# Kernel tuning notes

Measured on AMD Instinct MI355X. Metric: run time of the kernel, lower is better.

## Reference

```python
import jax, jax.numpy as jnp
import numpy as np

B, S, D = 4, 2048, 768
H, E = 12, 64  # num_heads, head_size


def setup_inputs() -> dict:
    key = jax.random.key(0)
    ks = jax.random.split(key, 9)
    sd = 1.0 / np.sqrt(D)
    return {
        "x": jax.random.normal(ks[0], (B, S, D), dtype=jnp.float32),
        "Wq": jax.random.normal(ks[1], (H, D, E), dtype=jnp.float32) * sd,
        "bq": jax.random.normal(ks[2], (H, E), dtype=jnp.float32) * 0.02,
        "Wk": jax.random.normal(ks[3], (H, D, E), dtype=jnp.float32) * sd,
        "bk": jax.random.normal(ks[4], (H, E), dtype=jnp.float32) * 0.02,
        "Wv": jax.random.normal(ks[5], (H, D, E), dtype=jnp.float32) * sd,
        "bv": jax.random.normal(ks[6], (H, E), dtype=jnp.float32) * 0.02,
        "Wp": jax.random.normal(ks[7], (H * E, D), dtype=jnp.float32) * sd,
        "bp": jax.random.normal(ks[8], (D,), dtype=jnp.float32) * 0.02,
    }


def reference(x, Wq, bq, Wk, bk, Wv, bv, Wp, bp):
    # Batched multi-head QKV projections (replaces per-head Python loop)
    q = jnp.einsum("bsd,hde->bhse", x, Wq) + bq[None, :, None, :]
    k = jnp.einsum("bsd,hde->bhse", x, Wk) + bk[None, :, None, :]
    v = jnp.einsum("bsd,hde->bhse", x, Wv) + bv[None, :, None, :]
    scale = 1.0 / jnp.sqrt(jnp.asarray(E, dtype=x.dtype))
    # Full materialized attention matrix [B,H,S,S] as in the original module
    wei = jnp.einsum("bhqe,bhke->bhqk", q, k) * scale
    wei = jax.nn.softmax(wei, axis=-1)  # dropout=0 (eval) => identity
    out = jnp.einsum("bhqk,bhke->bhqe", wei, v)  # [B,H,S,E]
    # concat heads in head order then output projection
    out = out.transpose(0, 2, 1, 3).reshape(B, S, H * E)
    return out @ Wp + bp
```

## Files before the change

### kernel.cpp

```cpp
#include <hip/hip_runtime.h>
#include <cstddef>
#include <cstdint>

#define NB 4
#define NH 12
#define SQ 2048
#define DM 768
#define EH 64
#define MTOT (NB*SQ)
#define NQKV (NH*3*EH)

typedef __attribute__((ext_vector_type(8))) short short8;
typedef __attribute__((ext_vector_type(4))) float floatx4;

#define QSCALE 0.18033688011112042f

__device__ __forceinline__ unsigned short f2bf(float f) {
    unsigned int u = __float_as_uint(f);
    u += 0x7fffu + ((u >> 16) & 1u);
    return (unsigned short)(u >> 16);
}

#if __has_builtin(__builtin_amdgcn_exp2f)
__device__ __forceinline__ float fast_exp2(float x) { return __builtin_amdgcn_exp2f(x); }
#else
__device__ __forceinline__ float fast_exp2(float x) { return exp2f(x); }
#endif

#if __has_builtin(__builtin_amdgcn_cvt_pk_bf16_f32)
typedef __attribute__((ext_vector_type(2))) __bf16 bf16x2_t;
__device__ __forceinline__ unsigned int pack_bf16(float lo, float hi) {
    bf16x2_t v = __builtin_amdgcn_cvt_pk_bf16_f32(lo, hi);
    return __builtin_bit_cast(unsigned int, v);
}
#else
__device__ __forceinline__ unsigned int pack_bf16(float lo, float hi) {
    unsigned int u0 = __float_as_uint(lo) + 0x8000u;
    unsigned int u1 = __float_as_uint(hi) + 0x8000u;
    return __builtin_amdgcn_perm(u1, u0, 0x07060302u);
}
#endif
__device__ __forceinline__ short8 pack8(float a0,float a1,float a2,float a3,
                                        float b0,float b1,float b2,float b3) {
    union { unsigned int u[4]; short8 s; } cv;
    cv.u[0] = pack_bf16(a0, a1);
    cv.u[1] = pack_bf16(a2, a3);
    cv.u[2] = pack_bf16(b0, b1);
    cv.u[3] = pack_bf16(b2, b3);
    return cv.s;
}
__device__ __forceinline__ void gl_lds16(const void* g, void* l) {
    __builtin_amdgcn_global_load_lds(
        (const __attribute__((address_space(1))) unsigned int*)g,
        (__attribute__((address_space(3))) unsigned int*)l, 16, 0, 0);
}

#define CVT_A 1572864
#define CVT_BIAS (CVT_A + 576)
#define NCVT ((CVT_BIAS + 255) / 256)
__global__ __launch_bounds__(256) void convert_all(
    const float* __restrict__ x,
    const float* __restrict__ Wq, const float* __restrict__ bq,
    const float* __restrict__ Wk, const float* __restrict__ bk,
    const float* __restrict__ Wv, const float* __restrict__ bv,
    const float* __restrict__ Wp,
    unsigned short* __restrict__ Xb, unsigned short* __restrict__ Wt,
    unsigned short* __restrict__ Wpt, float* __restrict__ bias_all)
{
    __shared__ unsigned short T[64][66];
    if (blockIdx.x < NCVT) {
        int t = blockIdx.x * 256 + threadIdx.x;
        if (t < CVT_A) {
            float4 v = ((const float4*)x)[t];
            ushort4 r; r.x = f2bf(v.x); r.y = f2bf(v.y); r.z = f2bf(v.z); r.w = f2bf(v.w);
            ((ushort4*)Xb)[t] = r;
        } else if (t < CVT_BIAS) {
            int u = (t - CVT_A) * 4;
            #pragma unroll
            for (int j = 0; j < 4; j++) {
                int n = u + j;
                int h = n / 192, rr = n % 192, wsel = rr >> 6, e = rr & 63;
                const float* bs = (wsel == 0) ? bq : ((wsel == 1) ? bk : bv);
                bias_all[n] = bs[h * EH + e] * ((wsel == 0) ? QSCALE : 1.0f);
            }
        }
        return;
    }
    const int bid = blockIdx.x - NCVT;
    const int t = threadIdx.x;
    const int rr = t >> 2;
    const int c4 = (t & 3) * 16;

    const float* src; int sstride; unsigned short* dst; float sc; int kt;
    if (bid < 432) {
        int j = bid / 12; kt = bid % 12;
        int h = j / 3, wsel = j % 3;
        const float* W = (wsel == 0) ? Wq : ((wsel == 1) ? Wk : Wv);
        src = W + (size_t)h * DM * EH;
        sstride = EH;
        dst = Wt + (size_t)(h * 192 + wsel * 64) * DM;
        sc = (wsel == 0) ? QSCALE : 1.0f;
    } else {
        int u = bid - 432;
        int ni = u / 12; kt = u % 12;
        src = Wp + ni * 64;
        sstride = DM;
        dst = Wpt + (size_t)(ni * 64) * DM;
        sc = 1.0f;
    }

    const float* s = src + (size_t)(kt * 64 + rr) * sstride + c4;
    #pragma unroll
    for (int j = 0; j < 16; j++)
        T[c4 + j][rr] = f2bf(s[j] * sc);
    __syncthreads();
    uint4 d0 = *(uint4*)&T[rr][c4];
    uint4 d1 = *(uint4*)&T[rr][c4 + 8];
    *(uint4*)&dst[(size_t)rr * DM + kt * 64 + c4]     = d0;
    *(uint4*)&dst[(size_t)rr * DM + kt * 64 + c4 + 8] = d1;
}

__global__ __launch_bounds__(256, 4) void qkv_mfma(
    const unsigned short* __restrict__ Xb, const unsigned short* __restrict__ Wt,
    const float* __restrict__ bias_all,
    unsigned short* __restrict__ Qo, unsigned short* __restrict__ Kf,
    unsigned short* __restrict__ Vf)
{
    __shared__ __align__(16) unsigned short SM[16384];
    unsigned short* const As0 = SM;
    unsigned short* const Bs0 = SM + 8192;
    const int tid = threadIdx.x;
    const int w = tid >> 6, lane = tid & 63;
    const int l15 = lane & 15, quad = lane >> 4;
    const int wm = w & 1, wn = w >> 1;
    const int lid = blockIdx.x + gridDim.x * blockIdx.y;
    const int xcd = lid & 7, pos = lid >> 3;
    const int bx = xcd * 8 + (pos & 7);
    const int by = pos >> 3;
    const int m0 = bx * 128, n0 = by * 128;
    const int srow = w * 32 + (lane >> 2);
    const int pchunk = lane & 3;

    floatx4 acc[4][4];
    #pragma unroll
    for (int i = 0; i < 4; i++)
        #pragma unroll
        for (int j = 0; j < 4; j++) acc[i][j] = 0;

    #pragma unroll
    for (int c = 0; c < 2; c++) {
        int mr = srow + c * 16;
        int j = (pchunk - (mr >> 1)) & 3;
        gl_lds16(&Xb[(size_t)(m0 + mr) * DM + j * 8],
                 &As0[w * 1024 + c * 512 + lane * 8]);
        gl_lds16(&Wt[(size_t)(n0 + mr) * DM + j * 8],
                 &Bs0[w * 1024 + c * 512 + lane * 8]);
    }

    for (int kt = 0; kt < DM / 32; kt++) {
        const int cur = kt & 1;
        __syncthreads();
        if (kt + 1 < DM / 32) {
            int k0n = (kt + 1) * 32;
            #pragma unroll
            for (int c = 0; c < 2; c++) {
                int mr = srow + c * 16;
                int j = (pchunk - (mr >> 1)) & 3;
                gl_lds16(&Xb[(size_t)(m0 + mr) * DM + k0n + j * 8],
                         &As0[(cur ^ 1) * 4096 + w * 1024 + c * 512 + lane * 8]);
                gl_lds16(&Wt[(size_t)(n0 + mr) * DM + k0n + j * 8],
                         &Bs0[(cur ^ 1) * 4096 + w * 1024 + c * 512 + lane * 8]);
            }
        }
        short8 af[4], bf[4];
        #pragma unroll
        for (int mi = 0; mi < 4; mi++) {
            int row = wm * 64 + mi * 16 + l15;
            int pp = (quad + (row >> 1)) & 3;
            af[mi] = *(const short8*)&As0[cur * 4096 + row * 32 + pp * 8];
        }
        #pragma unroll
        for (int ni = 0; ni < 4; ni++) {
            int row = wn * 64 + ni * 16 + l15;
            int pp = (quad + (row >> 1)) & 3;
            bf[ni] = *(const short8*)&Bs0[cur * 4096 + row * 32 + pp * 8];
        }
        #pragma unroll
        for (int mi = 0; mi < 4; mi++)
            #pragma unroll
            for (int ni = 0; ni < 4; ni++)
                acc[mi][ni] = __builtin_amdgcn_mfma_f32_16x16x32_bf16(
                    af[mi], bf[ni], acc[mi][ni], 0, 0, 0);
    }
    __syncthreads();

    const int bB = m0 >> 11;
    const int ntb0 = n0 + wn * 64;
    const int h = ntb0 / 192, rr = ntb0 % 192;
    const int wsel = rr >> 6;
    const size_t bhbase = ((size_t)bB * NH + h) * (SQ * EH);
    const int sb_base = (m0 & 2047) + wm * 64;
    unsigned short* Ew = SM + w * 1152;
    float bvv[4];
    #pragma unroll
    for (int ni = 0; ni < 4; ni++) bvv[ni] = bias_all[ntb0 + ni * 16 + l15];

    if (wsel == 0) {
        #pragma unroll
        for (int mi = 0; mi < 4; mi++) {
            #pragma unroll
            for (int ni = 0; ni < 4; ni++)
                #pragma unroll
                for (int r = 0; r < 4; r++)
                    Ew[(quad * 4 + r) * 72 + ni * 16 + l15] =
                        f2bf(acc[mi][ni][r] + bvv[ni]);
            #pragma unroll
            for (int t = 0; t < 2; t++) {
                uint4 d = *(uint4*)&Ew[(t * 8 + (lane >> 3)) * 72 + (lane & 7) * 8];
                *(uint4*)&Qo[bhbase +
                    (size_t)(sb_base + mi * 16 + t * 8 + (lane >> 3)) * EH +
                    (lane & 7) * 8] = d;
            }
        }
    } else if (wsel == 1) {
        size_t tbase = bhbase + (size_t)(sb_base >> 6) * 4096;
        #pragma unroll
        for (int mi = 0; mi < 4; mi++) {
            #pragma unroll
            for (int ni = 0; ni < 4; ni++)
                #pragma unroll
                for (int r = 0; r < 4; r++)
                    Ew[(quad * 4 + r) * 72 + ni * 16 + l15] =
                        f2bf(acc[mi][ni][r] + bvv[ni]);
            #pragma unroll
            for (int t = 0; t < 2; t++) {
                uint4 d = *(uint4*)&Ew[l15 * 72 + t * 32 + quad * 8];
                *(uint4*)&Kf[tbase +
                    (size_t)((mi * 2 + t) * 64 + quad * 16 + l15) * 8] = d;
            }
        }
    } else {
        size_t tbase = bhbase + (size_t)(sb_base >> 6) * 4096;
        #pragma unroll
        for (int ni = 0; ni < 4; ni++) {
            #pragma unroll
            for (int mi = 0; mi < 4; mi++)
                #pragma unroll
                for (int r = 0; r < 4; r += 2) {
                    unsigned int pr = pack_bf16(acc[mi][ni][r]     + bvv[ni],
                                                acc[mi][ni][r + 1] + bvv[ni]);
                    *(unsigned int*)&Ew[l15 * 72 + quad * 16 + mi * 4 + r] = pr;
                }
            #pragma unroll
            for (int t = 0; t < 2; t++) {
                uint4 d = *(uint4*)&Ew[l15 * 72 + t * 32 + quad * 8];
                int unit = (ni * 2 + (quad & 1)) * 64 + ((quad >> 1) + 2 * t) * 16 + l15;
                *(uint4*)&Vf[tbase + (size_t)unit * 8] = d;
            }
        }
    }
}

__global__ __launch_bounds__(256, 3) void attn_mfma(
    const unsigned short* __restrict__ Q, const unsigned short* __restrict__ Kf,
    const unsigned short* __restrict__ Vf, unsigned short* __restrict__ O)
{
    __shared__ unsigned short Ks[3 * 4096];
    __shared__ unsigned short Vs[3 * 4096];
    const int tid = threadIdx.x;
    const int w = tid >> 6, lane = tid & 63;
    const int l15 = lane & 15, quad = lane >> 4;
    const int bh = blockIdx.x;
    const int b = bh / NH, h = bh % NH;
    const int q0 = blockIdx.y * 128;
    const int lin = blockIdx.x + gridDim.x * blockIdx.y;
    const int t0 = (lin >> 8) * 11;

    const unsigned short* Qb = Q + (size_t)bh * SQ * EH;
    const unsigned short* Kb = Kf + (size_t)bh * SQ * EH;
    const unsigned short* Vb = Vf + (size_t)bh * SQ * EH;

    short8 qf[2][2];
    #pragma unroll
    for (int qh = 0; qh < 2; qh++)
        #pragma unroll
        for (int kh = 0; kh < 2; kh++)
            qf[qh][kh] = *(const short8*)
                &Qb[(size_t)(q0 + w * 32 + qh * 16 + l15) * EH + kh * 32 + quad * 8];

    short8 ones;
    #pragma unroll
    for (int j = 0; j < 8; j++) ones[j] = (short)0x3F80;
    const floatx4 fzero = 0;

    floatx4 o[2][4], l_acc[2];
    #pragma unroll
    for (int qh = 0; qh < 2; qh++) {
        l_acc[qh] = 0;
        #pragma unroll
        for (int nb = 0; nb < 4; nb++) o[qh][nb] = 0;
    }

    const int seg = w * 2;
    {
        const unsigned short* K0 = Kb + (size_t)t0 * 4096;
        const unsigned short* V0 = Vb + (size_t)t0 * 4096;
        #pragma unroll
        for (int c = 0; c < 2; c++) {
            gl_lds16(&K0[(seg + c) * 512 + lane * 8], &Ks[(seg + c) * 512 + lane * 8]);
            gl_lds16(&V0[(seg + c) * 512 + lane * 8], &Vs[(seg + c) * 512 + lane * 8]);
        }
    }
    asm volatile("" ::: "memory");
    {
        const int t1 = (t0 + 1) & 31;
        const unsigned short* K1 = Kb + (size_t)t1 * 4096;
        const unsigned short* V1 = Vb + (size_t)t1 * 4096;
        #pragma unroll
        for (int c = 0; c < 2; c++) {
            gl_lds16(&K1[(seg + c) * 512 + lane * 8],
                     &Ks[4096 + (seg + c) * 512 + lane * 8]);
            gl_lds16(&V1[(seg + c) * 512 + lane * 8],
                     &Vs[4096 + (seg + c) * 512 + lane * 8]);
        }
    }
    asm volatile("s_waitcnt vmcnt(4)\n\ts_barrier" ::: "memory");

    int cur_off = 0;
    for (int kb = 0; kb < SQ / 64; kb++) {
        if (kb + 2 < SQ / 64) {
            int nxt_off = cur_off + 8192;
            if (nxt_off >= 12288) nxt_off -= 12288;
            const int tt2 = (t0 + kb + 2) & 31;
            const unsigned short* Kn = Kb + (size_t)tt2 * 4096;
            const unsigned short* Vn = Vb + (size_t)tt2 * 4096;
            #pragma unroll
            for (int c = 0; c < 2; c++) {
                gl_lds16(&Kn[(seg + c) * 512 + lane * 8],
                         &Ks[nxt_off + (seg + c) * 512 + lane * 8]);
                gl_lds16(&Vn[(seg + c) * 512 + lane * 8],
                         &Vs[nxt_off + (seg + c) * 512 + lane * 8]);
            }
        }

        short8 kf[4][2], vf[4][2];
        #pragma unroll
        for (int nb = 0; nb < 4; nb++)
            #pragma unroll
            for (int kh = 0; kh < 2; kh++)
                kf[nb][kh] = *(const short8*)&Ks[cur_off + ((nb * 2 + kh) * 64 + lane) * 8];
        #pragma unroll
        for (int eb = 0; eb < 4; eb++)
            #pragma unroll
            for (int kh = 0; kh < 2; kh++)
                vf[eb][kh] = *(const short8*)&Vs[cur_off + ((eb * 2 + kh) * 64 + lane) * 8];

        floatx4 s[2][4];
        __builtin_amdgcn_s_setprio(1);
        #pragma unroll
        for (int qh = 0; qh < 2; qh++)
            #pragma unroll
            for (int nb = 0; nb < 4; nb++) {
                floatx4 z = __builtin_amdgcn_mfma_f32_16x16x32_bf16(
                    kf[nb][0], qf[qh][0], fzero, 0, 0, 0);
                s[qh][nb] = __builtin_amdgcn_mfma_f32_16x16x32_bf16(
                    kf[nb][1], qf[qh][1], z, 0, 0, 0);
            }
        __builtin_amdgcn_s_setprio(0);

        short8 pa[2][2];
        #pragma unroll
        for (int qh = 0; qh < 2; qh++) {
            float p[4][4];
            #pragma unroll
            for (int nb = 0; nb < 4; nb++)
                #pragma unroll
                for (int r = 0; r < 4; r++)
                    p[nb][r] = fast_exp2(s[qh][nb][r]);
            pa[qh][0] = pack8(p[0][0], p[0][1], p[0][2], p[0][3],
                              p[1][0], p[1][1], p[1][2], p[1][3]);
            pa[qh][1] = pack8(p[2][0], p[2][1], p[2][2], p[2][3],
                              p[3][0], p[3][1], p[3][2], p[3][3]);
        }

        __builtin_amdgcn_s_setprio(1);
        #pragma unroll
        for (int qh = 0; qh < 2; qh++) {
            l_acc[qh] = __builtin_amdgcn_mfma_f32_16x16x32_bf16(pa[qh][0], ones, l_acc[qh], 0, 0, 0);
            l_acc[qh] = __builtin_amdgcn_mfma_f32_16x16x32_bf16(pa[qh][1], ones, l_acc[qh], 0, 0, 0);
        }
        #pragma unroll
        for (int qh = 0; qh < 2; qh++)
            #pragma unroll
            for (int eb = 0; eb < 4; eb++) {
                o[qh][eb] = __builtin_amdgcn_mfma_f32_16x16x32_bf16(pa[qh][0], vf[eb][0], o[qh][eb], 0, 0, 0);
                o[qh][eb] = __builtin_amdgcn_mfma_f32_16x16x32_bf16(pa[qh][1], vf[eb][1], o[qh][eb], 0, 0, 0);
            }
        __builtin_amdgcn_s_setprio(0);

        if (kb + 2 < SQ / 64) {
            asm volatile("s_waitcnt vmcnt(4)\n\ts_barrier" ::: "memory");
        } else if (kb + 1 < SQ / 64) {
            asm volatile("s_waitcnt vmcnt(0)\n\ts_barrier" ::: "memory");
        }
        cur_off += 4096;
        if (cur_off >= 12288) cur_off = 0;
    }

    #pragma unroll
    for (int qh = 0; qh < 2; qh++)
        #pragma unroll
        for (int r = 0; r < 4; r++) {
            float inv = 1.0f / l_acc[qh][r];
            int sidx = q0 + w * 32 + qh * 16 + quad * 4 + r;
            size_t base = (((size_t)b * SQ + sidx) * NH + h) * EH + l15;
            O[base +  0] = f2bf(o[qh][0][r] * inv);
            O[base + 16] = f2bf(o[qh][1][r] * inv);
            O[base + 32] = f2bf(o[qh][2][r] * inv);
            O[base + 48] = f2bf(o[qh][3][r] * inv);
        }
}

__global__ __launch_bounds__(256, 3) void proj_mfma(
    const unsigned short* __restrict__ Ab, const unsigned short* __restrict__ Wpt,
    const float* __restrict__ bp, float* __restrict__ C)
{
    __shared__ __align__(16) unsigned short SM[24576];
    unsigned short* const As0 = SM;
    unsigned short* const Bs0 = SM + 8192;
    const int tid = threadIdx.x;
    const int w = tid >> 6, lane = tid & 63;
    const int l15 = lane & 15, quad = lane >> 4;
    const int wm = w & 1, wn = w >> 1;
    const int m0 = blockIdx.x * 64, n0 = blockIdx.y * 128;
    const int pchunk = lane & 3;

    floatx4 acc[2][4];
    #pragma unroll
    for (int i = 0; i < 2; i++)
        #pragma unroll
        for (int j = 0; j < 4; j++) acc[i][j] = 0;

    auto stage = [&](int kt, int buf) {
        #pragma unroll
        for (int kk = 0; kk < 2; kk++) {
            int k0 = kt * 64 + kk * 32;
            {
                int mr = w * 16 + (lane >> 2);
                int j = (pchunk - (mr >> 1)) & 3;
                gl_lds16(&Ab[(size_t)(m0 + mr) * DM + k0 + j * 8],
                         &As0[buf * 4096 + kk * 2048 + w * 512 + lane * 8]);
            }
            #pragma unroll
            for (int c = 0; c < 2; c++) {
                int nr = w * 32 + c * 16 + (lane >> 2);
                int j = (pchunk - (nr >> 1)) & 3;
                gl_lds16(&Wpt[(size_t)(n0 + nr) * DM + k0 + j * 8],
                         &Bs0[buf * 8192 + kk * 4096 + w * 1024 + c * 512 + lane * 8]);
            }
        }
    };

    stage(0, 0);

    for (int kt = 0; kt < DM / 64; kt++) {
        const int cur = kt & 1;
        __syncthreads();
        if (kt + 1 < DM / 64) stage(kt + 1, cur ^ 1);
        #pragma unroll
        for (int kk = 0; kk < 2; kk++) {
            short8 af[2], bf[4];
            #pragma unroll
            for (int mi = 0; mi < 2; mi++) {
                int row = wm * 32 + mi * 16 + l15;
                int pp = (quad + (row >> 1)) & 3;
                af[mi] = *(const short8*)
                    &As0[cur * 4096 + kk * 2048 + row * 32 + pp * 8];
            }
            #pragma unroll
            for (int ni = 0; ni < 4; ni++) {
                int row = wn * 64 + ni * 16 + l15;
                int pp = (quad + (row >> 1)) & 3;
                bf[ni] = *(const short8*)
                    &Bs0[cur * 8192 + kk * 4096 + row * 32 + pp * 8];
            }
            #pragma unroll
            for (int mi = 0; mi < 2; mi++)
                #pragma unroll
                for (int ni = 0; ni < 4; ni++)
                    acc[mi][ni] = __builtin_amdgcn_mfma_f32_16x16x32_bf16(
                        af[mi], bf[ni], acc[mi][ni], 0, 0, 0);
        }
    }
    __syncthreads();

    float* const Ewf = (float*)SM + w * 1088;
    float bvv[4];
    #pragma unroll
    for (int ni = 0; ni < 4; ni++) bvv[ni] = bp[n0 + wn * 64 + ni * 16 + l15];
    #pragma unroll
    for (int mi = 0; mi < 2; mi++) {
        #pragma unroll
        for (int ni = 0; ni < 4; ni++)
            #pragma unroll
            for (int r = 0; r < 4; r++)
                Ewf[(quad * 4 + r) * 68 + ni * 16 + l15] = acc[mi][ni][r] + bvv[ni];
        #pragma unroll
        for (int t = 0; t < 4; t++) {
            float4 d = *(float4*)&Ewf[(t * 4 + quad) * 68 + l15 * 4];
            *(float4*)&C[(size_t)(m0 + wm * 32 + mi * 16 + t * 4 + quad) * DM +
                         n0 + wn * 64 + l15 * 4] = d;
        }
    }
}

extern "C" void kernel_launch(void* const* d_in, const int* in_sizes, int n_in,
                              void* d_out, int out_size, void* d_ws, size_t ws_size,
                              hipStream_t stream) {
    const float* x  = (const float*)d_in[0];
    const float* Wq = (const float*)d_in[1];
    const float* bq = (const float*)d_in[2];
    const float* Wk = (const float*)d_in[3];
    const float* bk = (const float*)d_in[4];
    const float* Wv = (const float*)d_in[5];
    const float* bv = (const float*)d_in[6];
    const float* Wp = (const float*)d_in[7];
    const float* bp = (const float*)d_in[8];
    float* out = (float*)d_out;

    const size_t QKV_ELEMS = (size_t)NB * NH * SQ * EH;
    unsigned short* Qb   = (unsigned short*)d_ws;
    unsigned short* Kfb  = Qb + QKV_ELEMS;
    unsigned short* Vfb  = Kfb + QKV_ELEMS;
    unsigned short* Abuf = Vfb + QKV_ELEMS;
    unsigned short* Xb   = Abuf + QKV_ELEMS;
    unsigned short* Wtb  = Xb + QKV_ELEMS;
    unsigned short* Wptb = Wtb + (size_t)NQKV * DM;
    float* bias_all      = (float*)(Wptb + (size_t)DM * DM);

    convert_all<<<NCVT + 576, 256, 0, stream>>>(
        x, Wq, bq, Wk, bk, Wv, bv, Wp, Xb, Wtb, Wptb, bias_all);
    qkv_mfma<<<dim3(MTOT / 128, NQKV / 128), 256, 0, stream>>>(
        Xb, Wtb, bias_all, Qb, Kfb, Vfb);
    attn_mfma<<<dim3(NB * NH, SQ / 128), 256, 0, stream>>>(Qb, Kfb, Vfb, Abuf);
    proj_mfma<<<dim3(MTOT / 64, DM / 128), 256, 0, stream>>>(Abuf, Wptb, bp, out);
}
```

Baseline: 208.0 us.

## Load K/V fragments directly from global memory instead of LDS triple-buffer

Removes the shared-memory triple-buffered async K/V staging, its barriers and the staggered tile start. Each wave now reads its K and V MFMA fragments straight from global memory (through L2/L1) every iteration. Launch bounds occupancy is raised from 3 to 6 blocks per CU to hide the added load latency. In exchange, each of the four waves in a block now issues its own redundant global loads for the same tile, the loads are exposed with no prefetch, and all blocks of a head walk the same tiles in lockstep instead of staggered.

```diff
diff --git a/kernel.cpp b/kernel.cpp
--- a/kernel.cpp
+++ b/kernel.cpp
@@ -261,20 +261,16 @@
     }
 }
 
-__global__ __launch_bounds__(256, 3) void attn_mfma(
+__global__ __launch_bounds__(256, 6) void attn_mfma(
     const unsigned short* __restrict__ Q, const unsigned short* __restrict__ Kf,
     const unsigned short* __restrict__ Vf, unsigned short* __restrict__ O)
 {
-    __shared__ unsigned short Ks[3 * 4096];
-    __shared__ unsigned short Vs[3 * 4096];
     const int tid = threadIdx.x;
     const int w = tid >> 6, lane = tid & 63;
     const int l15 = lane & 15, quad = lane >> 4;
     const int bh = blockIdx.x;
     const int b = bh / NH, h = bh % NH;
     const int q0 = blockIdx.y * 128;
-    const int lin = blockIdx.x + gridDim.x * blockIdx.y;
-    const int t0 = (lin >> 8) * 11;
 
     const unsigned short* Qb = Q + (size_t)bh * SQ * EH;
     const unsigned short* Kb = Kf + (size_t)bh * SQ * EH;
@@ -301,59 +297,20 @@
         for (int nb = 0; nb < 4; nb++) o[qh][nb] = 0;
     }
 
-    const int seg = w * 2;
-    {
-        const unsigned short* K0 = Kb + (size_t)t0 * 4096;
-        const unsigned short* V0 = Vb + (size_t)t0 * 4096;
-        #pragma unroll
-        for (int c = 0; c < 2; c++) {
-            gl_lds16(&K0[(seg + c) * 512 + lane * 8], &Ks[(seg + c) * 512 + lane * 8]);
-            gl_lds16(&V0[(seg + c) * 512 + lane * 8], &Vs[(seg + c) * 512 + lane * 8]);
-        }
-    }
-    asm volatile("" ::: "memory");
-    {
-        const int t1 = (t0 + 1) & 31;
-        const unsigned short* K1 = Kb + (size_t)t1 * 4096;
-        const unsigned short* V1 = Vb + (size_t)t1 * 4096;
-        #pragma unroll
-        for (int c = 0; c < 2; c++) {
-            gl_lds16(&K1[(seg + c) * 512 + lane * 8],
-                     &Ks[4096 + (seg + c) * 512 + lane * 8]);
-            gl_lds16(&V1[(seg + c) * 512 + lane * 8],
-                     &Vs[4096 + (seg + c) * 512 + lane * 8]);
-        }
-    }
-    asm volatile("s_waitcnt vmcnt(4)\n\ts_barrier" ::: "memory");
-
-    int cur_off = 0;
     for (int kb = 0; kb < SQ / 64; kb++) {
-        if (kb + 2 < SQ / 64) {
-            int nxt_off = cur_off + 8192;
-            if (nxt_off >= 12288) nxt_off -= 12288;
-            const int tt2 = (t0 + kb + 2) & 31;
-            const unsigned short* Kn = Kb + (size_t)tt2 * 4096;
-            const unsigned short* Vn = Vb + (size_t)tt2 * 4096;
-            #pragma unroll
-            for (int c = 0; c < 2; c++) {
-                gl_lds16(&Kn[(seg + c) * 512 + lane * 8],
-                         &Ks[nxt_off + (seg + c) * 512 + lane * 8]);
-                gl_lds16(&Vn[(seg + c) * 512 + lane * 8],
-                         &Vs[nxt_off + (seg + c) * 512 + lane * 8]);
-            }
-        }
-
+        const unsigned short* Kt = Kb + (size_t)kb * 4096;
+        const unsigned short* Vt = Vb + (size_t)kb * 4096;
         short8 kf[4][2], vf[4][2];
         #pragma unroll
         for (int nb = 0; nb < 4; nb++)
             #pragma unroll
             for (int kh = 0; kh < 2; kh++)
-                kf[nb][kh] = *(const short8*)&Ks[cur_off + ((nb * 2 + kh) * 64 + lane) * 8];
+                kf[nb][kh] = *(const short8*)&Kt[((nb * 2 + kh) * 64 + lane) * 8];
         #pragma unroll
         for (int eb = 0; eb < 4; eb++)
             #pragma unroll
             for (int kh = 0; kh < 2; kh++)
-                vf[eb][kh] = *(const short8*)&Vs[cur_off + ((eb * 2 + kh) * 64 + lane) * 8];
+                vf[eb][kh] = *(const short8*)&Vt[((eb * 2 + kh) * 64 + lane) * 8];
 
         floatx4 s[2][4];
         __builtin_amdgcn_s_setprio(1);
@@ -397,14 +354,6 @@
                 o[qh][eb] = __builtin_amdgcn_mfma_f32_16x16x32_bf16(pa[qh][1], vf[eb][1], o[qh][eb], 0, 0, 0);
             }
         __builtin_amdgcn_s_setprio(0);
-
-        if (kb + 2 < SQ / 64) {
-            asm volatile("s_waitcnt vmcnt(4)\n\ts_barrier" ::: "memory");
-        } else if (kb + 1 < SQ / 64) {
-            asm volatile("s_waitcnt vmcnt(0)\n\ts_barrier" ::: "memory");
-        }
-        cur_off += 4096;
-        if (cur_off >= 12288) cur_off = 0;
     }
 
     #pragma unroll
```

Result: slower. 601.7 us (+189.3%).
